# Performance work log

Measured on AMD Instinct MI355X. Metric: run time of the kernel, lower is better.

Reference implementation:

```python
import jax, jax.numpy as jnp
import numpy as np

B, N, D, U = 8, 4096, 128, 1024


def setup_inputs() -> dict:
    key = jax.random.key(0)
    kx, kw = jax.random.split(key)
    x = jax.random.normal(kx, (B, N, D), dtype=jnp.float32)
    # learned kernel, shape (dims, units) as in build()
    w = jax.random.normal(kw, (D, U), dtype=jnp.float32)
    return {"x": x, "w": w}


def reference(x, w):
    # Squared Euclidean distance from every point x[b,n,:] to every prototype
    # column w[:,u]: sum_d (x[b,n,d] - w[d,u])^2.
    # work is a single GEMM instead of materializing a [B,N,D,U] tensor.
    x2 = jnp.sum(x * x, axis=-1, keepdims=True)        # [B, N, 1]
    w2 = jnp.sum(w * w, axis=0)                        # [U]
    xw = jnp.einsum("bnd,du->bnu", x, w)               # [B, N, U]
    a = x2 + w2 - 2.0 * xw                             # [B, N, U]
    # inverted=False, activation=None -> return raw squared distances
    return a
```

## Files before the change

### kernel.cpp

```cpp
#include <hip/hip_runtime.h>

#define M_TOT 32768
#define K_DIM 128
#define U_TOT 1024

#define BM 128
#define BN 128
#define BK 32

typedef short s16x8 __attribute__((ext_vector_type(8)));
typedef float f32x4 __attribute__((ext_vector_type(4)));

__device__ inline unsigned int f2bf(float f) {
    union { float f; unsigned int u; } v; v.f = f;
    unsigned int r = v.u + 0x7FFFu + ((v.u >> 16) & 1u);
    return r >> 16;
}

__device__ inline void async_load16(const void* g, void* l) {
    __builtin_amdgcn_global_load_lds((const __attribute__((address_space(1))) void*)g,
                                     (__attribute__((address_space(3))) void*)l,
                                     16, 0, 0);
}

__global__ __launch_bounds__(256) void prep_kernel(
    const float* __restrict__ x, const float* __restrict__ w,
    unsigned int* __restrict__ xb, unsigned int* __restrict__ wt,
    float* __restrict__ x2, float* __restrict__ w2)
{
    const int lane = threadIdx.x & 63;
    const int gw = (blockIdx.x << 2) + (threadIdx.x >> 6);
    if (gw < M_TOT) {
        const float2 v = ((const float2*)(x + (size_t)gw * K_DIM))[lane];
        float s = v.x * v.x + v.y * v.y;
        #pragma unroll
        for (int off = 32; off; off >>= 1) s += __shfl_xor(s, off);
        xb[gw * 64 + lane] = f2bf(v.x) | (f2bf(v.y) << 16);
        if (lane == 0) x2[gw] = s;
    } else if (gw < M_TOT + U_TOT) {
        const int u = gw - M_TOT;
        const float a = w[(size_t)(2 * lane) * U_TOT + u];
        const float b = w[(size_t)(2 * lane + 1) * U_TOT + u];
        float s = a * a + b * b;
        #pragma unroll
        for (int off = 32; off; off >>= 1) s += __shfl_xor(s, off);
        wt[u * 64 + lane] = f2bf(a) | (f2bf(b) << 16);
        if (lane == 0) w2[u] = s;
    }
}

__global__ __launch_bounds__(256) void gemm_kernel(
    const unsigned short* __restrict__ xb, const unsigned short* __restrict__ wt,
    const float* __restrict__ x2, const float* __restrict__ w2,
    float* __restrict__ out)
{
    __shared__ __align__(16) unsigned short As[BM * BK];
    __shared__ __align__(16) unsigned short Bs[BN * BK];

    const int tid = threadIdx.x;
    const int wv = tid >> 6;
    const int lane = tid & 63;
    const int m0 = (int)(blockIdx.x >> 3) * BM;
    const int u0 = (int)(blockIdx.x & 7) * BN;
    const int wm = (wv & 1) * 64;
    const int wn = (wv >> 1) * 64;
    const int col = lane & 15;
    const int quad = lane >> 4;
    const int srow = lane >> 2;
    const int sch = (lane & 3) * 8;

    f32x4 acc[4][4] = {};

    #pragma unroll
    for (int kt = 0; kt < 4; ++kt) {
        const int k0 = kt * BK;
        #pragma unroll
        for (int i = 0; i < 2; ++i) {
            const int rb = (wv * 2 + i) * 16;
            async_load16(xb + (size_t)(m0 + rb + srow) * K_DIM + k0 + sch, &As[rb * BK]);
            async_load16(wt + (size_t)(u0 + rb + srow) * K_DIM + k0 + sch, &Bs[rb * BK]);
        }
        __syncthreads();

        s16x8 af[4], bfr[4];
        #pragma unroll
        for (int t = 0; t < 4; ++t) {
            af[t]  = *(const s16x8*)&As[(wm + t * 16 + col) * BK + quad * 8];
            bfr[t] = *(const s16x8*)&Bs[(wn + t * 16 + col) * BK + quad * 8];
        }
        #pragma unroll
        for (int a = 0; a < 4; ++a)
            #pragma unroll
            for (int b = 0; b < 4; ++b)
                acc[a][b] = __builtin_amdgcn_mfma_f32_16x16x32_bf16(af[a], bfr[b], acc[a][b], 0, 0, 0);
        __syncthreads();
    }

    const int orow = quad * 4;
    #pragma unroll
    for (int a = 0; a < 4; ++a) {
        const int mb = m0 + wm + a * 16 + orow;
        float xs[4];
        #pragma unroll
        for (int r = 0; r < 4; ++r) xs[r] = x2[mb + r];
        #pragma unroll
        for (int b = 0; b < 4; ++b) {
            const int u = u0 + wn + b * 16 + col;
            const float wsq = w2[u];
            float* op = out + (size_t)mb * U_TOT + u;
            #pragma unroll
            for (int r = 0; r < 4; ++r)
                op[(size_t)r * U_TOT] = xs[r] + wsq - 2.0f * acc[a][b][r];
        }
    }
}

__global__ __launch_bounds__(256) void fallback_kernel(
    const float* __restrict__ x, const float* __restrict__ w,
    float* __restrict__ out)
{
    __shared__ float xrow[K_DIM];
    const int m = blockIdx.x;
    const int tid = threadIdx.x;
    if (tid < K_DIM) xrow[tid] = x[(size_t)m * K_DIM + tid];
    __syncthreads();
    float x2 = 0.f;
    #pragma unroll
    for (int k = 0; k < K_DIM; ++k) x2 += xrow[k] * xrow[k];
    #pragma unroll
    for (int uu = 0; uu < 4; ++uu) {
        const int u = uu * 256 + tid;
        float dot = 0.f, w2 = 0.f;
        for (int k = 0; k < K_DIM; ++k) {
            const float wv = w[(size_t)k * U_TOT + u];
            dot += xrow[k] * wv;
            w2 += wv * wv;
        }
        out[(size_t)m * U_TOT + u] = x2 + w2 - 2.0f * dot;
    }
}

extern "C" void kernel_launch(void* const* d_in, const int* in_sizes, int n_in,
                              void* d_out, int out_size, void* d_ws, size_t ws_size,
                              hipStream_t stream) {
    const float* x = (const float*)d_in[0];
    const float* w = (const float*)d_in[1];
    float* out = (float*)d_out;

    const size_t need = (size_t)M_TOT * K_DIM * 2 + (size_t)U_TOT * K_DIM * 2
                      + (size_t)M_TOT * 4 + (size_t)U_TOT * 4;
    if (ws_size < need) {
        fallback_kernel<<<M_TOT, 256, 0, stream>>>(x, w, out);
        return;
    }

    unsigned short* xb = (unsigned short*)d_ws;
    unsigned short* wt = xb + (size_t)M_TOT * K_DIM;
    float* x2 = (float*)(wt + (size_t)U_TOT * K_DIM);
    float* w2 = x2 + M_TOT;

    prep_kernel<<<(M_TOT + U_TOT) / 4, 256, 0, stream>>>(x, w, (unsigned int*)xb,
                                                         (unsigned int*)wt, x2, w2);
    gemm_kernel<<<(M_TOT / BM) * (U_TOT / BN), 256, 0, stream>>>(xb, wt, x2, w2, out);
}
```

Before: 160.4 us.

## Fuse x conversion and norm into GEMM, load full K tile with swizzled LDS

```diff
diff --git a/kernel.cpp b/kernel.cpp
--- a/kernel.cpp
+++ b/kernel.cpp
@@ -3,18 +3,15 @@
 #define M_TOT 32768
 #define K_DIM 128
 #define U_TOT 1024
-
 #define BM 128
 #define BN 128
-#define BK 32
 
 typedef short s16x8 __attribute__((ext_vector_type(8)));
 typedef float f32x4 __attribute__((ext_vector_type(4)));
 
 __device__ inline unsigned int f2bf(float f) {
     union { float f; unsigned int u; } v; v.f = f;
-    unsigned int r = v.u + 0x7FFFu + ((v.u >> 16) & 1u);
-    return r >> 16;
+    return (v.u + 0x7FFFu + ((v.u >> 16) & 1u)) >> 16;
 }
 
 __device__ inline void async_load16(const void* g, void* l) {
@@ -23,94 +20,107 @@
                                      16, 0, 0);
 }
 
-__global__ __launch_bounds__(256) void prep_kernel(
-    const float* __restrict__ x, const float* __restrict__ w,
-    unsigned int* __restrict__ xb, unsigned int* __restrict__ wt,
-    float* __restrict__ x2, float* __restrict__ w2)
+__device__ inline int swz(int row, int j) { return (row << 4) | (j ^ (row & 15)); }
+
+__global__ __launch_bounds__(256) void prep_w(
+    const float* __restrict__ w, unsigned int* __restrict__ wt, float* __restrict__ w2)
 {
     const int lane = threadIdx.x & 63;
-    const int gw = (blockIdx.x << 2) + (threadIdx.x >> 6);
-    if (gw < M_TOT) {
-        const float2 v = ((const float2*)(x + (size_t)gw * K_DIM))[lane];
-        float s = v.x * v.x + v.y * v.y;
-        #pragma unroll
-        for (int off = 32; off; off >>= 1) s += __shfl_xor(s, off);
-        xb[gw * 64 + lane] = f2bf(v.x) | (f2bf(v.y) << 16);
-        if (lane == 0) x2[gw] = s;
-    } else if (gw < M_TOT + U_TOT) {
-        const int u = gw - M_TOT;
-        const float a = w[(size_t)(2 * lane) * U_TOT + u];
-        const float b = w[(size_t)(2 * lane + 1) * U_TOT + u];
-        float s = a * a + b * b;
-        #pragma unroll
-        for (int off = 32; off; off >>= 1) s += __shfl_xor(s, off);
-        wt[u * 64 + lane] = f2bf(a) | (f2bf(b) << 16);
-        if (lane == 0) w2[u] = s;
-    }
+    const int u = (blockIdx.x << 2) + (threadIdx.x >> 6);
+    const float a = w[(size_t)(2 * lane) * U_TOT + u];
+    const float b = w[(size_t)(2 * lane + 1) * U_TOT + u];
+    float s = a * a + b * b;
+    #pragma unroll
+    for (int off = 32; off; off >>= 1) s += __shfl_xor(s, off);
+    wt[u * 64 + lane] = f2bf(a) | (f2bf(b) << 16);
+    if (lane == 0) w2[u] = s;
 }
 
-__global__ __launch_bounds__(256) void gemm_kernel(
-    const unsigned short* __restrict__ xb, const unsigned short* __restrict__ wt,
-    const float* __restrict__ x2, const float* __restrict__ w2,
-    float* __restrict__ out)
+__global__ __launch_bounds__(256, 2) void gemm_kernel(
+    const float* __restrict__ x, const unsigned short* __restrict__ wt,
+    const float* __restrict__ w2, float* __restrict__ out)
 {
-    __shared__ __align__(16) unsigned short As[BM * BK];
-    __shared__ __align__(16) unsigned short Bs[BN * BK];
+    __shared__ __align__(16) unsigned short As[BM * K_DIM];
+    __shared__ __align__(16) unsigned short Bs[BN * K_DIM];
 
     const int tid = threadIdx.x;
     const int wv = tid >> 6;
     const int lane = tid & 63;
-    const int m0 = (int)(blockIdx.x >> 3) * BM;
-    const int u0 = (int)(blockIdx.x & 7) * BN;
-    const int wm = (wv & 1) * 64;
-    const int wn = (wv >> 1) * 64;
+
+    const int b = blockIdx.x;
+    const int mt = (b & 7) * 32 + ((b >> 3) >> 3);
+    const int ut = (b >> 3) & 7;
+    const int m0 = mt * BM;
+    const int u0 = ut * BN;
+
+    #pragma unroll
+    for (int i = 0; i < 8; ++i) {
+        const int p = i * 256 + tid;
+        const int row = p >> 4;
+        const int j = (p & 15) ^ (row & 15);
+        async_load16(wt + ((size_t)(u0 + row) << 7) + j * 8,
+                     &Bs[(i * 256 + (tid & 192)) * 8]);
+    }
+
+    const int ar = tid >> 1;
+    const int ah = tid & 1;
+    const float4* xs4 = (const float4*)(x + ((size_t)(m0 + ar) << 7) + (ah << 6));
+    float ssum = 0.f;
+    #pragma unroll
+    for (int c = 0; c < 8; ++c) {
+        const float4 v0 = xs4[2 * c];
+        const float4 v1 = xs4[2 * c + 1];
+        ssum += v0.x * v0.x + v0.y * v0.y + v0.z * v0.z + v0.w * v0.w
+              + v1.x * v1.x + v1.y * v1.y + v1.z * v1.z + v1.w * v1.w;
+        uint4 pk;
+        pk.x = f2bf(v0.x) | (f2bf(v0.y) << 16);
+        pk.y = f2bf(v0.z) | (f2bf(v0.w) << 16);
+        pk.z = f2bf(v1.x) | (f2bf(v1.y) << 16);
+        pk.w = f2bf(v1.z) | (f2bf(v1.w) << 16);
+        *(uint4*)&As[swz(ar, (ah << 3) + c) * 8] = pk;
+    }
+    ssum += __shfl_xor(ssum, 1);
+
+    __syncthreads();
+
     const int col = lane & 15;
     const int quad = lane >> 4;
-    const int srow = lane >> 2;
-    const int sch = (lane & 3) * 8;
+    const int wm = wv << 5;
 
-    f32x4 acc[4][4] = {};
-
+    f32x4 acc[2][8] = {};
     #pragma unroll
-    for (int kt = 0; kt < 4; ++kt) {
-        const int k0 = kt * BK;
+    for (int kk = 0; kk < 4; ++kk) {
+        const int jj = (kk << 2) + quad;
+        s16x8 af[2], bfr[8];
         #pragma unroll
-        for (int i = 0; i < 2; ++i) {
-            const int rb = (wv * 2 + i) * 16;
-            async_load16(xb + (size_t)(m0 + rb + srow) * K_DIM + k0 + sch, &As[rb * BK]);
-            async_load16(wt + (size_t)(u0 + rb + srow) * K_DIM + k0 + sch, &Bs[rb * BK]);
-        }
-        __syncthreads();
-
-        s16x8 af[4], bfr[4];
+        for (int a = 0; a < 2; ++a)
+            af[a] = *(const s16x8*)&As[swz(wm + a * 16 + col, jj) * 8];
         #pragma unroll
-        for (int t = 0; t < 4; ++t) {
-            af[t]  = *(const s16x8*)&As[(wm + t * 16 + col) * BK + quad * 8];
-            bfr[t] = *(const s16x8*)&Bs[(wn + t * 16 + col) * BK + quad * 8];
-        }
+        for (int n = 0; n < 8; ++n)
+            bfr[n] = *(const s16x8*)&Bs[swz(n * 16 + col, jj) * 8];
         #pragma unroll
-        for (int a = 0; a < 4; ++a)
+        for (int a = 0; a < 2; ++a)
             #pragma unroll
-            for (int b = 0; b < 4; ++b)
-                acc[a][b] = __builtin_amdgcn_mfma_f32_16x16x32_bf16(af[a], bfr[b], acc[a][b], 0, 0, 0);
-        __syncthreads();
+            for (int n = 0; n < 8; ++n)
+                acc[a][n] = __builtin_amdgcn_mfma_f32_16x16x32_bf16(af[a], bfr[n], acc[a][n], 0, 0, 0);
     }
 
-    const int orow = quad * 4;
+    const int orow = quad << 2;
     #pragma unroll
-    for (int a = 0; a < 4; ++a) {
-        const int mb = m0 + wm + a * 16 + orow;
-        float xs[4];
+    for (int a = 0; a < 2; ++a) {
+        const int lr = wm + a * 16 + orow;
+        float xsq[4];
         #pragma unroll
-        for (int r = 0; r < 4; ++r) xs[r] = x2[mb + r];
+        for (int r = 0; r < 4; ++r)
+            xsq[r] = __shfl(ssum, (a * 16 + orow + r) << 1);
         #pragma unroll
-        for (int b = 0; b < 4; ++b) {
-            const int u = u0 + wn + b * 16 + col;
+        for (int n = 0; n < 8; ++n) {
+            const int u = u0 + n * 16 + col;
             const float wsq = w2[u];
-            float* op = out + (size_t)mb * U_TOT + u;
+            float* op = out + (size_t)(m0 + lr) * U_TOT + u;
             #pragma unroll
             for (int r = 0; r < 4; ++r)
-                op[(size_t)r * U_TOT] = xs[r] + wsq - 2.0f * acc[a][b][r];
+                op[(size_t)r * U_TOT] = xsq[r] + wsq - 2.0f * acc[a][n][r];
         }
     }
 }
@@ -147,19 +157,15 @@
     const float* w = (const float*)d_in[1];
     float* out = (float*)d_out;
 
-    const size_t need = (size_t)M_TOT * K_DIM * 2 + (size_t)U_TOT * K_DIM * 2
-                      + (size_t)M_TOT * 4 + (size_t)U_TOT * 4;
+    const size_t need = (size_t)U_TOT * K_DIM * 2 + (size_t)U_TOT * 4;
     if (ws_size < need) {
         fallback_kernel<<<M_TOT, 256, 0, stream>>>(x, w, out);
         return;
     }
 
-    unsigned short* xb = (unsigned short*)d_ws;
-    unsigned short* wt = xb + (size_t)M_TOT * K_DIM;
-    float* x2 = (float*)(wt + (size_t)U_TOT * K_DIM);
-    float* w2 = x2 + M_TOT;
+    unsigned short* wt = (unsigned short*)d_ws;
+    float* w2 = (float*)(wt + (size_t)U_TOT * K_DIM);
 
-    prep_kernel<<<(M_TOT + U_TOT) / 4, 256, 0, stream>>>(x, w, (unsigned int*)xb,
-                                                         (unsigned int*)wt, x2, w2);
-    gemm_kernel<<<(M_TOT / BM) * (U_TOT / BN), 256, 0, stream>>>(xb, wt, x2, w2, out);
+    prep_w<<<U_TOT / 4, 256, 0, stream>>>(w, (unsigned int*)wt, w2);
+    gemm_kernel<<<(M_TOT / BM) * (U_TOT / BN), 256, 0, stream>>>(x, wt, w2, out);
 }
```

After: 166.1 us. 3.5% more time.
